# Kernel optimization log

Hardware: AMD Instinct MI355X
Metric: run time of the kernel (lower is better)

The kernel has to match this reference:

```python
import jax, jax.numpy as jnp
import numpy as np


def _gather_neighbours(h, idx):
    # h: (B, N, H); idx: (B, N, K) int -> (B, N, K, H)
    B, N, H = h.shape
    K = idx.shape[-1]
    flat = idx.reshape(B, N * K)  # (B, N*K)
    rep = jnp.take_along_axis(h, flat[..., None], axis=1)  # (B, N*K, H)
    return rep.reshape(B, N, K, H)


def _masked_agg(h, idx, mask):
    # gather neighbor hidden states then masked sum over neighbors -> (B, N, H)
    rep = _gather_neighbours(h, idx)
    return jnp.einsum('bnkh,bnk->bnh', rep, mask)


def setup_inputs() -> dict:
    key = jax.random.key(0)
    ks = jax.random.split(key, 12)
    B, N, H, K = 8, 2000, 128, 32
    s = 1.0 / np.sqrt(H)
    return {
        'node_hidden': jax.random.normal(ks[0], (B, N, H), jnp.float32),
        'cell': jax.random.normal(ks[1], (B, N, H), jnp.float32),
        'w_in': jax.random.normal(ks[2], (4, H, H), jnp.float32) * s,
        'w_out': jax.random.normal(ks[3], (4, H, H), jnp.float32) * s,
        'u_in': jax.random.normal(ks[4], (4, H, H), jnp.float32) * s,
        'u_out': jax.random.normal(ks[5], (4, H, H), jnp.float32) * s,
        'b': jax.random.normal(ks[6], (4, H), jnp.float32) * 0.1,
        'in_node_mask': jax.random.uniform(ks[7], (B, N, K), jnp.float32),
        'out_node_mask': jax.random.uniform(ks[8], (B, N, K), jnp.float32),
        'in_node_index': jax.random.randint(ks[9], (B, N, K), 0, N, jnp.int32),
        'out_node_index': jax.random.randint(ks[10], (B, N, K), 0, N, jnp.int32),
        'layer_num': 2,
    }


def reference(node_hidden, cell, w_in, w_out, u_in, u_out, b,
              in_node_mask, out_node_mask, in_node_index, out_node_index,
              layer_num):
    h, c = node_hidden, cell
    for _ in range(layer_num):
        in_agg = _masked_agg(h, in_node_index, in_node_mask)    # (B,N,H)
        out_agg = _masked_agg(h, out_node_index, out_node_mask)  # (B,N,H)
        # gate pre-activations, gate order: i, o, f, cell
        pre = (jnp.einsum('bnh,ghd->gbnd', in_agg, w_in)
               + jnp.einsum('bnh,ghd->gbnd', out_agg, w_out)
               + jnp.einsum('bnh,ghd->gbnd', h, u_in)
               + jnp.einsum('bnh,ghd->gbnd', h, u_out)
               + b[:, None, None, :])
        i_g = jax.nn.sigmoid(pre[0])
        o_g = jax.nn.sigmoid(pre[1])
        f_g = jax.nn.sigmoid(pre[2])
        g = jnp.tanh(pre[3])
        c = f_g * c + i_g * g
        h = o_g * jnp.tanh(c)
    return h
```

## Files before the change

kernel.cpp:

```cpp
#include <hip/hip_runtime.h>
#include <math.h>

#define B_ 8
#define N_ 2000
#define H_ 128
#define K_ 32
#define M_ (B_*N_)
#define KTOT 384
#define NC 512

typedef __attribute__((ext_vector_type(8))) short s8_t;
typedef __attribute__((ext_vector_type(4))) float f4_t;

__device__ __forceinline__ unsigned short f2bf(float x) {
    union { float f; unsigned u; } v; v.f = x;
    unsigned r = v.u + 0x7fff + ((v.u >> 16) & 1);
    return (unsigned short)(r >> 16);
}
__device__ __forceinline__ float bf2f(unsigned short b) {
    union { unsigned u; float f; } v; v.u = (unsigned)b << 16; return v.f;
}
__device__ __forceinline__ float sigm_(float x) { return 1.f / (1.f + __expf(-x)); }
__device__ __forceinline__ float tanh_(float x) { return 2.f / (1.f + __expf(-2.f * x)) - 1.f; }

__device__ __forceinline__ float pickv(f4_t A, int m) {
    float ab = (m & 1) ? A.y : A.x;
    float cd = (m & 1) ? A.w : A.z;
    return (m & 2) ? cd : ab;
}
__device__ __forceinline__ float pick4(float u0, float u1, float u2, float u3, int m) {
    float ab = (m & 1) ? u1 : u0;
    float cd = (m & 1) ? u3 : u2;
    return (m & 2) ? cd : ab;
}

__device__ __forceinline__ void cvt8(float4 a, float4 b, uint4& hi, uint4& lo) {
    float f[8] = {a.x, a.y, a.z, a.w, b.x, b.y, b.z, b.w};
    unsigned h[8], l[8];
    #pragma unroll
    for (int i = 0; i < 8; ++i) {
        unsigned short hs = f2bf(f[i]);
        h[i] = hs;
        l[i] = f2bf(f[i] - bf2f(hs));
    }
    hi.x = h[0] | (h[1] << 16); hi.y = h[2] | (h[3] << 16);
    hi.z = h[4] | (h[5] << 16); hi.w = h[6] | (h[7] << 16);
    lo.x = l[0] | (l[1] << 16); lo.y = l[2] | (l[3] << 16);
    lo.z = l[4] | (l[5] << 16); lo.w = l[6] | (l[7] << 16);
}

__global__ void prep_kernel(const float* __restrict__ w_in,
                            const float* __restrict__ w_out,
                            const float* __restrict__ u_in,
                            const float* __restrict__ u_out,
                            unsigned short* __restrict__ wp_hi,
                            unsigned short* __restrict__ wp_lo) {
    int j = blockIdx.x;
    int k = threadIdx.x;
    int d = j >> 2, g = j & 3;
    float v;
    if (k < 128) {
        v = w_in[(g * 128 + k) * 128 + d];
    } else if (k < 256) {
        v = w_out[(g * 128 + (k - 128)) * 128 + d];
    } else {
        int kk = k - 256;
        v = u_in[(g * 128 + kk) * 128 + d] + u_out[(g * 128 + kk) * 128 + d];
    }
    unsigned short hs = f2bf(v);
    wp_hi[(size_t)j * KTOT + k] = hs;
    wp_lo[(size_t)j * KTOT + k] = f2bf(v - bf2f(hs));
}

__global__ __launch_bounds__(256)
void agg_kernel(const float* __restrict__ h,
                const int* __restrict__ in_idx,
                const float* __restrict__ in_mask,
                const int* __restrict__ out_idx,
                const float* __restrict__ out_mask,
                unsigned short* __restrict__ agg_hi,
                unsigned short* __restrict__ agg_lo) {
    int tid = threadIdx.x;
    int r = tid >> 5;
    int t = tid & 31;
    int row = blockIdx.x * 8 + r;
    int b = row / N_;
    const float* hb = h + (size_t)b * N_ * H_;

    __shared__ int   s_idx[8][64];
    __shared__ float s_msk[8][64];
    for (int e = tid; e < 512; e += 256) {
        int r2 = e >> 6, q = e & 63;
        int ridx = blockIdx.x * 8 + r2;
        if (q < 32) {
            s_idx[r2][q] = in_idx[ridx * K_ + q];
            s_msk[r2][q] = in_mask[ridx * K_ + q];
        } else {
            s_idx[r2][q] = out_idx[ridx * K_ + (q - 32)];
            s_msk[r2][q] = out_mask[ridx * K_ + (q - 32)];
        }
    }
    __syncthreads();

    float ax = 0.f, ay = 0.f, az = 0.f, aw = 0.f;
    float ox = 0.f, oy = 0.f, oz = 0.f, ow = 0.f;
    #pragma unroll 4
    for (int k = 0; k < K_; ++k) {
        int   i1 = s_idx[r][k];
        float m1 = s_msk[r][k];
        float4 v1 = *(const float4*)(hb + (size_t)i1 * H_ + t * 4);
        int   i2 = s_idx[r][32 + k];
        float m2 = s_msk[r][32 + k];
        float4 v2 = *(const float4*)(hb + (size_t)i2 * H_ + t * 4);
        ax += m1 * v1.x; ay += m1 * v1.y; az += m1 * v1.z; aw += m1 * v1.w;
        ox += m2 * v2.x; oy += m2 * v2.y; oz += m2 * v2.z; ow += m2 * v2.w;
    }

    float fi[4] = {ax, ay, az, aw};
    float fo[4] = {ox, oy, oz, ow};
    unsigned short hi_i[4], lo_i[4], hi_o[4], lo_o[4];
    #pragma unroll
    for (int q = 0; q < 4; ++q) {
        hi_i[q] = f2bf(fi[q]); lo_i[q] = f2bf(fi[q] - bf2f(hi_i[q]));
        hi_o[q] = f2bf(fo[q]); lo_o[q] = f2bf(fo[q] - bf2f(hi_o[q]));
    }
    size_t base = (size_t)row * 256;
    *(ushort4*)(agg_hi + base + t * 4)       = make_ushort4(hi_i[0], hi_i[1], hi_i[2], hi_i[3]);
    *(ushort4*)(agg_lo + base + t * 4)       = make_ushort4(lo_i[0], lo_i[1], lo_i[2], lo_i[3]);
    *(ushort4*)(agg_hi + base + 128 + t * 4) = make_ushort4(hi_o[0], hi_o[1], hi_o[2], hi_o[3]);
    *(ushort4*)(agg_lo + base + 128 + t * 4) = make_ushort4(lo_o[0], lo_o[1], lo_o[2], lo_o[3]);
}

__global__ __launch_bounds__(256)
void gemm_gates(const unsigned short* __restrict__ agg_hi,
                const unsigned short* __restrict__ agg_lo,
                const float* __restrict__ h_src,
                const unsigned short* __restrict__ wp_hi,
                const unsigned short* __restrict__ wp_lo,
                const float* __restrict__ bias,
                const float* __restrict__ c_src,
                float* __restrict__ c_dst,
                float* __restrict__ h_dst) {
    __shared__ short As_hi[128 * 32];
    __shared__ short As_lo[128 * 32];
    __shared__ short Ws_hi[128 * 32];
    __shared__ short Ws_lo[128 * 32];

    int tid  = threadIdx.x;
    int mt   = blockIdx.x;
    int jt   = blockIdx.y;
    int row0 = mt * 128;
    int lane = tid & 63;
    int wave = tid >> 6;
    int m_off = (wave & 1) * 64;
    int n_off = (wave >> 1) * 64;
    int ml = lane & 15;
    int kg = lane >> 4;

    f4_t zero = {0.f, 0.f, 0.f, 0.f};
    f4_t acc[4][4];
    #pragma unroll
    for (int i = 0; i < 4; ++i)
        #pragma unroll
        for (int j = 0; j < 4; ++j) acc[i][j] = zero;

    int e0 = tid, e1 = tid + 256;
    int ar0 = e0 >> 2, ac0 = e0 & 3;
    int ar1 = e1 >> 2, ac1 = e1 & 3;

    #pragma unroll 1
    for (int k0 = 0; k0 < KTOT; k0 += 32) {
        uint4 ahi0, alo0, ahi1, alo1;
        if (k0 < 256) {
            const unsigned short* ph = agg_hi + (size_t)row0 * 256 + k0;
            const unsigned short* pl = agg_lo + (size_t)row0 * 256 + k0;
            ahi0 = *(const uint4*)(ph + ar0 * 256 + ac0 * 8);
            alo0 = *(const uint4*)(pl + ar0 * 256 + ac0 * 8);
            ahi1 = *(const uint4*)(ph + ar1 * 256 + ac1 * 8);
            alo1 = *(const uint4*)(pl + ar1 * 256 + ac1 * 8);
        } else {
            const float* pf = h_src + (size_t)row0 * 128 + (k0 - 256);
            float4 f0a = *(const float4*)(pf + ar0 * 128 + ac0 * 8);
            float4 f0b = *(const float4*)(pf + ar0 * 128 + ac0 * 8 + 4);
            float4 f1a = *(const float4*)(pf + ar1 * 128 + ac1 * 8);
            float4 f1b = *(const float4*)(pf + ar1 * 128 + ac1 * 8 + 4);
            cvt8(f0a, f0b, ahi0, alo0);
            cvt8(f1a, f1b, ahi1, alo1);
        }
        const unsigned short* pwh = wp_hi + (size_t)(jt * 128) * KTOT + k0;
        const unsigned short* pwl = wp_lo + (size_t)(jt * 128) * KTOT + k0;
        uint4 whi0 = *(const uint4*)(pwh + ar0 * KTOT + ac0 * 8);
        uint4 wlo0 = *(const uint4*)(pwl + ar0 * KTOT + ac0 * 8);
        uint4 whi1 = *(const uint4*)(pwh + ar1 * KTOT + ac1 * 8);
        uint4 wlo1 = *(const uint4*)(pwl + ar1 * KTOT + ac1 * 8);

        __syncthreads();
        *(uint4*)&As_hi[e0 * 8] = ahi0;
        *(uint4*)&As_hi[e1 * 8] = ahi1;
        *(uint4*)&As_lo[e0 * 8] = alo0;
        *(uint4*)&As_lo[e1 * 8] = alo1;
        *(uint4*)&Ws_hi[e0 * 8] = whi0;
        *(uint4*)&Ws_hi[e1 * 8] = whi1;
        *(uint4*)&Ws_lo[e0 * 8] = wlo0;
        *(uint4*)&Ws_lo[e1 * 8] = wlo1;
        __syncthreads();

        s8_t a_hi[4], a_lo[4], b_hi[4], b_lo[4];
        #pragma unroll
        for (int i = 0; i < 4; ++i) {
            int m = m_off + i * 16 + ml;
            a_hi[i] = *(const s8_t*)&As_hi[m * 32 + kg * 8];
            a_lo[i] = *(const s8_t*)&As_lo[m * 32 + kg * 8];
        }
        #pragma unroll
        for (int j = 0; j < 4; ++j) {
            int n = n_off + j * 16 + ml;
            b_hi[j] = *(const s8_t*)&Ws_hi[n * 32 + kg * 8];
            b_lo[j] = *(const s8_t*)&Ws_lo[n * 32 + kg * 8];
        }
        #pragma unroll
        for (int i = 0; i < 4; ++i)
            #pragma unroll
            for (int j = 0; j < 4; ++j) {
                acc[i][j] = __builtin_amdgcn_mfma_f32_16x16x32_bf16(a_hi[i], b_hi[j], acc[i][j], 0, 0, 0);
                acc[i][j] = __builtin_amdgcn_mfma_f32_16x16x32_bf16(a_hi[i], b_lo[j], acc[i][j], 0, 0, 0);
                acc[i][j] = __builtin_amdgcn_mfma_f32_16x16x32_bf16(a_lo[i], b_hi[j], acc[i][j], 0, 0, 0);
            }
    }

    int g    = lane & 3;
    int qrow = lane >> 4;
    int dl   = (lane >> 2) & 3;
    #pragma unroll
    for (int j = 0; j < 4; ++j) {
        int ncol_base = jt * 128 + n_off + j * 16;
        int d = (ncol_base >> 2) + dl;
        float b0 = bias[0 * 128 + d];
        float b1 = bias[1 * 128 + d];
        float b2 = bias[2 * 128 + d];
        float b3 = bias[3 * 128 + d];
        #pragma unroll
        for (int i = 0; i < 4; ++i) {
            f4_t A = acc[i][j];
            float s0 = pickv(A, g);
            float s1 = pickv(A, g ^ 1);
            float s2 = pickv(A, g ^ 2);
            float s3 = pickv(A, g ^ 3);
            float u0 = s0;
            float u1 = __shfl_xor(s1, 1);
            float u2 = __shfl_xor(s2, 2);
            float u3 = __shfl_xor(s3, 3);
            float p0 = pick4(u0, u1, u2, u3, g) + b0;
            float p1 = pick4(u0, u1, u2, u3, g ^ 1) + b1;
            float p2 = pick4(u0, u1, u2, u3, g ^ 2) + b2;
            float p3 = pick4(u0, u1, u2, u3, g ^ 3) + b3;
            float ig = sigm_(p0);
            float og = sigm_(p1);
            float fg = sigm_(p2);
            float cg = tanh_(p3);
            int row = row0 + m_off + i * 16 + qrow * 4 + g;
            size_t off = (size_t)row * H_ + d;
            float c_old = c_src[off];
            float c_new = fg * c_old + ig * cg;
            c_dst[off] = c_new;
            h_dst[off] = og * tanh_(c_new);
        }
    }
}

extern "C" void kernel_launch(void* const* d_in, const int* in_sizes, int n_in,
                              void* d_out, int out_size, void* d_ws, size_t ws_size,
                              hipStream_t stream) {
    const float* node_hidden = (const float*)d_in[0];
    const float* cell        = (const float*)d_in[1];
    const float* w_in        = (const float*)d_in[2];
    const float* w_out       = (const float*)d_in[3];
    const float* u_in        = (const float*)d_in[4];
    const float* u_out       = (const float*)d_in[5];
    const float* bias        = (const float*)d_in[6];
    const float* in_mask     = (const float*)d_in[7];
    const float* out_mask    = (const float*)d_in[8];
    const int*   in_idx      = (const int*)d_in[9];
    const int*   out_idx     = (const int*)d_in[10];
    float* out = (float*)d_out;

    char* p = (char*)d_ws;
    unsigned short* wp_hi  = (unsigned short*)p;                     p += (size_t)NC * KTOT * 2;
    unsigned short* wp_lo  = (unsigned short*)p;                     p += (size_t)NC * KTOT * 2;
    unsigned short* agg_hi = (unsigned short*)p;                     p += (size_t)M_ * 256 * 2;
    unsigned short* agg_lo = (unsigned short*)p;                     p += (size_t)M_ * 256 * 2;
    float* h_buf = (float*)p;                                        p += (size_t)M_ * H_ * 4;
    float* c_buf = (float*)p;                                        p += (size_t)M_ * H_ * 4;

    prep_kernel<<<NC, KTOT, 0, stream>>>(w_in, w_out, u_in, u_out, wp_hi, wp_lo);

    agg_kernel<<<M_ / 8, 256, 0, stream>>>(node_hidden, in_idx, in_mask,
                                           out_idx, out_mask, agg_hi, agg_lo);
    gemm_gates<<<dim3(M_ / 128, 4), 256, 0, stream>>>(
        agg_hi, agg_lo, node_hidden, wp_hi, wp_lo, bias, cell, c_buf, h_buf);

    agg_kernel<<<M_ / 8, 256, 0, stream>>>(h_buf, in_idx, in_mask,
                                           out_idx, out_mask, agg_hi, agg_lo);
    gemm_gates<<<dim3(M_ / 128, 4), 256, 0, stream>>>(
        agg_hi, agg_lo, h_buf, wp_hi, wp_lo, bias, c_buf, c_buf, out);
}
```

Measured before the change: 205.8 us.

## Fuse neighbour aggregation and gate GEMM into one per-layer kernel

Merges the gather-aggregate kernel and the gate GEMM into a single kernel per layer. Each 32-row block aggregates in/out neighbours and h into LDS as split bf16 hi/lo, then multiplies against all 512 gate columns. Weights are prepacked into the MFMA fragment order so they can be read straight from global memory without LDS staging. This removes the global round trip of the aggregated activations and two launches, in exchange for smaller M tiles, weight traffic repeated across 500 blocks, and higher register pressure.

```diff
diff --git a/kernel.cpp b/kernel.cpp
--- a/kernel.cpp
+++ b/kernel.cpp
@@ -8,6 +8,8 @@
 #define M_ (B_*N_)
 #define KTOT 384
 #define NC 512
+#define NTILES 32
+#define NCHUNK 12
 
 typedef __attribute__((ext_vector_type(8))) short s8_t;
 typedef __attribute__((ext_vector_type(4))) float f4_t;
@@ -34,8 +36,7 @@
     return (m & 2) ? cd : ab;
 }
 
-__device__ __forceinline__ void cvt8(float4 a, float4 b, uint4& hi, uint4& lo) {
-    float f[8] = {a.x, a.y, a.z, a.w, b.x, b.y, b.z, b.w};
+__device__ __forceinline__ void split_store(short* ph, short* pl, const float* f) {
     unsigned h[8], l[8];
     #pragma unroll
     for (int i = 0; i < 8; ++i) {
@@ -43,21 +44,29 @@
         h[i] = hs;
         l[i] = f2bf(f[i] - bf2f(hs));
     }
-    hi.x = h[0] | (h[1] << 16); hi.y = h[2] | (h[3] << 16);
-    hi.z = h[4] | (h[5] << 16); hi.w = h[6] | (h[7] << 16);
-    lo.x = l[0] | (l[1] << 16); lo.y = l[2] | (l[3] << 16);
-    lo.z = l[4] | (l[5] << 16); lo.w = l[6] | (l[7] << 16);
-}
-
-__global__ void prep_kernel(const float* __restrict__ w_in,
-                            const float* __restrict__ w_out,
-                            const float* __restrict__ u_in,
-                            const float* __restrict__ u_out,
-                            unsigned short* __restrict__ wp_hi,
-                            unsigned short* __restrict__ wp_lo) {
-    int j = blockIdx.x;
-    int k = threadIdx.x;
-    int d = j >> 2, g = j & 3;
+    uint4 H, L;
+    H.x = h[0] | (h[1] << 16); H.y = h[2] | (h[3] << 16);
+    H.z = h[4] | (h[5] << 16); H.w = h[6] | (h[7] << 16);
+    L.x = l[0] | (l[1] << 16); L.y = l[2] | (l[3] << 16);
+    L.z = l[4] | (l[5] << 16); L.w = l[6] | (l[7] << 16);
+    *(uint4*)ph = H;
+    *(uint4*)pl = L;
+}
+
+__global__ __launch_bounds__(512)
+void prep_kernel(const float* __restrict__ w_in,
+                 const float* __restrict__ w_out,
+                 const float* __restrict__ u_in,
+                 const float* __restrict__ u_out,
+                 unsigned short* __restrict__ wp_hi,
+                 unsigned short* __restrict__ wp_lo) {
+    int blk = blockIdx.x;
+    int ntile = blk / NCHUNK, chunk = blk % NCHUNK;
+    int t = threadIdx.x;
+    int lane = t >> 3, e = t & 7;
+    int col = ntile * 16 + (lane & 15);
+    int k = chunk * 32 + (lane >> 4) * 8 + e;
+    int d = col >> 2, g = col & 3;
     float v;
     if (k < 128) {
         v = w_in[(g * 128 + k) * 128 + d];
@@ -68,164 +77,109 @@
         v = u_in[(g * 128 + kk) * 128 + d] + u_out[(g * 128 + kk) * 128 + d];
     }
     unsigned short hs = f2bf(v);
-    wp_hi[(size_t)j * KTOT + k] = hs;
-    wp_lo[(size_t)j * KTOT + k] = f2bf(v - bf2f(hs));
-}
-
-__global__ __launch_bounds__(256)
-void agg_kernel(const float* __restrict__ h,
-                const int* __restrict__ in_idx,
-                const float* __restrict__ in_mask,
-                const int* __restrict__ out_idx,
-                const float* __restrict__ out_mask,
-                unsigned short* __restrict__ agg_hi,
-                unsigned short* __restrict__ agg_lo) {
+    wp_hi[(size_t)blk * 512 + t] = hs;
+    wp_lo[(size_t)blk * 512 + t] = f2bf(v - bf2f(hs));
+}
+
+__global__ __launch_bounds__(512, 4)
+void fused_layer(const float* __restrict__ h_src,
+                 const int* __restrict__ in_idx,
+                 const float* __restrict__ in_mask,
+                 const int* __restrict__ out_idx,
+                 const float* __restrict__ out_mask,
+                 const unsigned short* __restrict__ wp_hi,
+                 const unsigned short* __restrict__ wp_lo,
+                 const float* __restrict__ bias,
+                 const float* __restrict__ c_src,
+                 float* __restrict__ c_dst,
+                 float* __restrict__ h_dst) {
+    __shared__ short As_hi[NCHUNK * 32 * 32];
+    __shared__ short As_lo[NCHUNK * 32 * 32];
+
     int tid = threadIdx.x;
-    int r = tid >> 5;
-    int t = tid & 31;
-    int row = blockIdx.x * 8 + r;
-    int b = row / N_;
-    const float* hb = h + (size_t)b * N_ * H_;
-
-    __shared__ int   s_idx[8][64];
-    __shared__ float s_msk[8][64];
-    for (int e = tid; e < 512; e += 256) {
-        int r2 = e >> 6, q = e & 63;
-        int ridx = blockIdx.x * 8 + r2;
-        if (q < 32) {
-            s_idx[r2][q] = in_idx[ridx * K_ + q];
-            s_msk[r2][q] = in_mask[ridx * K_ + q];
-        } else {
-            s_idx[r2][q] = out_idx[ridx * K_ + (q - 32)];
-            s_msk[r2][q] = out_mask[ridx * K_ + (q - 32)];
-        }
+    int row0 = blockIdx.x * 32;
+
+    {
+        int r = tid >> 4;
+        int p = tid & 15;
+        int d0 = p * 8;
+        int row = row0 + r;
+        int b = row / N_;
+        const float* hb = h_src + (size_t)b * N_ * H_;
+        const int*   pii = in_idx  + (size_t)row * K_;
+        const float* pim = in_mask + (size_t)row * K_;
+        const int*   poi = out_idx + (size_t)row * K_;
+        const float* pom = out_mask + (size_t)row * K_;
+
+        float ai[8] = {0,0,0,0,0,0,0,0};
+        float ao[8] = {0,0,0,0,0,0,0,0};
+        #pragma unroll 4
+        for (int k = 0; k < K_; ++k) {
+            int   ii = pii[k];
+            float mi = pim[k];
+            int   oi = poi[k];
+            float mo = pom[k];
+            const float* pv = hb + (size_t)ii * H_ + d0;
+            const float* pw = hb + (size_t)oi * H_ + d0;
+            float4 v0 = *(const float4*)pv;
+            float4 v1 = *(const float4*)(pv + 4);
+            float4 w0 = *(const float4*)pw;
+            float4 w1 = *(const float4*)(pw + 4);
+            ai[0] += mi * v0.x; ai[1] += mi * v0.y; ai[2] += mi * v0.z; ai[3] += mi * v0.w;
+            ai[4] += mi * v1.x; ai[5] += mi * v1.y; ai[6] += mi * v1.z; ai[7] += mi * v1.w;
+            ao[0] += mo * w0.x; ao[1] += mo * w0.y; ao[2] += mo * w0.z; ao[3] += mo * w0.w;
+            ao[4] += mo * w1.x; ao[5] += mo * w1.y; ao[6] += mo * w1.z; ao[7] += mo * w1.w;
+        }
+        const float* ph = h_src + (size_t)row * H_ + d0;
+        float4 u0 = *(const float4*)ph;
+        float4 u1 = *(const float4*)(ph + 4);
+        float hh[8] = {u0.x, u0.y, u0.z, u0.w, u1.x, u1.y, u1.z, u1.w};
+
+        int ci  = p >> 2;
+        int off = (p & 3) * 8;
+        int base_in = ((ci)     * 32 + r) * 32 + off;
+        int base_ou = ((4 + ci) * 32 + r) * 32 + off;
+        int base_hh = ((8 + ci) * 32 + r) * 32 + off;
+        split_store(&As_hi[base_in], &As_lo[base_in], ai);
+        split_store(&As_hi[base_ou], &As_lo[base_ou], ao);
+        split_store(&As_hi[base_hh], &As_lo[base_hh], hh);
     }
     __syncthreads();
 
-    float ax = 0.f, ay = 0.f, az = 0.f, aw = 0.f;
-    float ox = 0.f, oy = 0.f, oz = 0.f, ow = 0.f;
-    #pragma unroll 4
-    for (int k = 0; k < K_; ++k) {
-        int   i1 = s_idx[r][k];
-        float m1 = s_msk[r][k];
-        float4 v1 = *(const float4*)(hb + (size_t)i1 * H_ + t * 4);
-        int   i2 = s_idx[r][32 + k];
-        float m2 = s_msk[r][32 + k];
-        float4 v2 = *(const float4*)(hb + (size_t)i2 * H_ + t * 4);
-        ax += m1 * v1.x; ay += m1 * v1.y; az += m1 * v1.z; aw += m1 * v1.w;
-        ox += m2 * v2.x; oy += m2 * v2.y; oz += m2 * v2.z; ow += m2 * v2.w;
-    }
-
-    float fi[4] = {ax, ay, az, aw};
-    float fo[4] = {ox, oy, oz, ow};
-    unsigned short hi_i[4], lo_i[4], hi_o[4], lo_o[4];
-    #pragma unroll
-    for (int q = 0; q < 4; ++q) {
-        hi_i[q] = f2bf(fi[q]); lo_i[q] = f2bf(fi[q] - bf2f(hi_i[q]));
-        hi_o[q] = f2bf(fo[q]); lo_o[q] = f2bf(fo[q] - bf2f(hi_o[q]));
-    }
-    size_t base = (size_t)row * 256;
-    *(ushort4*)(agg_hi + base + t * 4)       = make_ushort4(hi_i[0], hi_i[1], hi_i[2], hi_i[3]);
-    *(ushort4*)(agg_lo + base + t * 4)       = make_ushort4(lo_i[0], lo_i[1], lo_i[2], lo_i[3]);
-    *(ushort4*)(agg_hi + base + 128 + t * 4) = make_ushort4(hi_o[0], hi_o[1], hi_o[2], hi_o[3]);
-    *(ushort4*)(agg_lo + base + 128 + t * 4) = make_ushort4(lo_o[0], lo_o[1], lo_o[2], lo_o[3]);
-}
-
-__global__ __launch_bounds__(256)
-void gemm_gates(const unsigned short* __restrict__ agg_hi,
-                const unsigned short* __restrict__ agg_lo,
-                const float* __restrict__ h_src,
-                const unsigned short* __restrict__ wp_hi,
-                const unsigned short* __restrict__ wp_lo,
-                const float* __restrict__ bias,
-                const float* __restrict__ c_src,
-                float* __restrict__ c_dst,
-                float* __restrict__ h_dst) {
-    __shared__ short As_hi[128 * 32];
-    __shared__ short As_lo[128 * 32];
-    __shared__ short Ws_hi[128 * 32];
-    __shared__ short Ws_lo[128 * 32];
-
-    int tid  = threadIdx.x;
-    int mt   = blockIdx.x;
-    int jt   = blockIdx.y;
-    int row0 = mt * 128;
     int lane = tid & 63;
-    int wave = tid >> 6;
-    int m_off = (wave & 1) * 64;
-    int n_off = (wave >> 1) * 64;
+    int w = tid >> 6;
     int ml = lane & 15;
     int kg = lane >> 4;
 
     f4_t zero = {0.f, 0.f, 0.f, 0.f};
-    f4_t acc[4][4];
+    f4_t acc[2][4];
     #pragma unroll
-    for (int i = 0; i < 4; ++i)
+    for (int i = 0; i < 2; ++i)
         #pragma unroll
         for (int j = 0; j < 4; ++j) acc[i][j] = zero;
 
-    int e0 = tid, e1 = tid + 256;
-    int ar0 = e0 >> 2, ac0 = e0 & 3;
-    int ar1 = e1 >> 2, ac1 = e1 & 3;
-
-    #pragma unroll 1
-    for (int k0 = 0; k0 < KTOT; k0 += 32) {
-        uint4 ahi0, alo0, ahi1, alo1;
-        if (k0 < 256) {
-            const unsigned short* ph = agg_hi + (size_t)row0 * 256 + k0;
-            const unsigned short* pl = agg_lo + (size_t)row0 * 256 + k0;
-            ahi0 = *(const uint4*)(ph + ar0 * 256 + ac0 * 8);
-            alo0 = *(const uint4*)(pl + ar0 * 256 + ac0 * 8);
-            ahi1 = *(const uint4*)(ph + ar1 * 256 + ac1 * 8);
-            alo1 = *(const uint4*)(pl + ar1 * 256 + ac1 * 8);
-        } else {
-            const float* pf = h_src + (size_t)row0 * 128 + (k0 - 256);
-            float4 f0a = *(const float4*)(pf + ar0 * 128 + ac0 * 8);
-            float4 f0b = *(const float4*)(pf + ar0 * 128 + ac0 * 8 + 4);
-            float4 f1a = *(const float4*)(pf + ar1 * 128 + ac1 * 8);
-            float4 f1b = *(const float4*)(pf + ar1 * 128 + ac1 * 8 + 4);
-            cvt8(f0a, f0b, ahi0, alo0);
-            cvt8(f1a, f1b, ahi1, alo1);
-        }
-        const unsigned short* pwh = wp_hi + (size_t)(jt * 128) * KTOT + k0;
-        const unsigned short* pwl = wp_lo + (size_t)(jt * 128) * KTOT + k0;
-        uint4 whi0 = *(const uint4*)(pwh + ar0 * KTOT + ac0 * 8);
-        uint4 wlo0 = *(const uint4*)(pwl + ar0 * KTOT + ac0 * 8);
-        uint4 whi1 = *(const uint4*)(pwh + ar1 * KTOT + ac1 * 8);
-        uint4 wlo1 = *(const uint4*)(pwl + ar1 * KTOT + ac1 * 8);
-
-        __syncthreads();
-        *(uint4*)&As_hi[e0 * 8] = ahi0;
-        *(uint4*)&As_hi[e1 * 8] = ahi1;
-        *(uint4*)&As_lo[e0 * 8] = alo0;
-        *(uint4*)&As_lo[e1 * 8] = alo1;
-        *(uint4*)&Ws_hi[e0 * 8] = whi0;
-        *(uint4*)&Ws_hi[e1 * 8] = whi1;
-        *(uint4*)&Ws_lo[e0 * 8] = wlo0;
-        *(uint4*)&Ws_lo[e1 * 8] = wlo1;
-        __syncthreads();
-
-        s8_t a_hi[4], a_lo[4], b_hi[4], b_lo[4];
-        #pragma unroll
-        for (int i = 0; i < 4; ++i) {
-            int m = m_off + i * 16 + ml;
-            a_hi[i] = *(const s8_t*)&As_hi[m * 32 + kg * 8];
-            a_lo[i] = *(const s8_t*)&As_lo[m * 32 + kg * 8];
+    int w4 = w * 4;
+    #pragma unroll 2
+    for (int c = 0; c < NCHUNK; ++c) {
+        s8_t a_hi[2], a_lo[2];
+        #pragma unroll
+        for (int i = 0; i < 2; ++i) {
+            int m = i * 16 + ml;
+            a_hi[i] = *(const s8_t*)&As_hi[(c * 32 + m) * 32 + kg * 8];
+            a_lo[i] = *(const s8_t*)&As_lo[(c * 32 + m) * 32 + kg * 8];
         }
         #pragma unroll
         for (int j = 0; j < 4; ++j) {
-            int n = n_off + j * 16 + ml;
-            b_hi[j] = *(const s8_t*)&Ws_hi[n * 32 + kg * 8];
-            b_lo[j] = *(const s8_t*)&Ws_lo[n * 32 + kg * 8];
-        }
-        #pragma unroll
-        for (int i = 0; i < 4; ++i)
+            size_t boff = (((size_t)(w4 + j) * NCHUNK + c) * 64 + lane) * 8;
+            s8_t b_hi = *(const s8_t*)(wp_hi + boff);
+            s8_t b_lo = *(const s8_t*)(wp_lo + boff);
             #pragma unroll
-            for (int j = 0; j < 4; ++j) {
-                acc[i][j] = __builtin_amdgcn_mfma_f32_16x16x32_bf16(a_hi[i], b_hi[j], acc[i][j], 0, 0, 0);
-                acc[i][j] = __builtin_amdgcn_mfma_f32_16x16x32_bf16(a_hi[i], b_lo[j], acc[i][j], 0, 0, 0);
-                acc[i][j] = __builtin_amdgcn_mfma_f32_16x16x32_bf16(a_lo[i], b_hi[j], acc[i][j], 0, 0, 0);
+            for (int i = 0; i < 2; ++i) {
+                acc[i][j] = __builtin_amdgcn_mfma_f32_16x16x32_bf16(a_hi[i], b_hi, acc[i][j], 0, 0, 0);
+                acc[i][j] = __builtin_amdgcn_mfma_f32_16x16x32_bf16(a_hi[i], b_lo, acc[i][j], 0, 0, 0);
+                acc[i][j] = __builtin_amdgcn_mfma_f32_16x16x32_bf16(a_lo[i], b_hi, acc[i][j], 0, 0, 0);
             }
+        }
     }
 
     int g    = lane & 3;
@@ -233,14 +187,14 @@
     int dl   = (lane >> 2) & 3;
     #pragma unroll
     for (int j = 0; j < 4; ++j) {
-        int ncol_base = jt * 128 + n_off + j * 16;
+        int ncol_base = w * 64 + j * 16;
         int d = (ncol_base >> 2) + dl;
         float b0 = bias[0 * 128 + d];
         float b1 = bias[1 * 128 + d];
         float b2 = bias[2 * 128 + d];
         float b3 = bias[3 * 128 + d];
         #pragma unroll
-        for (int i = 0; i < 4; ++i) {
+        for (int i = 0; i < 2; ++i) {
             f4_t A = acc[i][j];
             float s0 = pickv(A, g);
             float s1 = pickv(A, g ^ 1);
@@ -258,7 +212,7 @@
             float og = sigm_(p1);
             float fg = sigm_(p2);
             float cg = tanh_(p3);
-            int row = row0 + m_off + i * 16 + qrow * 4 + g;
+            int row = row0 + i * 16 + qrow * 4 + g;
             size_t off = (size_t)row * H_ + d;
             float c_old = c_src[off];
             float c_new = fg * c_old + ig * cg;
@@ -285,22 +239,18 @@
     float* out = (float*)d_out;
 
     char* p = (char*)d_ws;
-    unsigned short* wp_hi  = (unsigned short*)p;                     p += (size_t)NC * KTOT * 2;
-    unsigned short* wp_lo  = (unsigned short*)p;                     p += (size_t)NC * KTOT * 2;
-    unsigned short* agg_hi = (unsigned short*)p;                     p += (size_t)M_ * 256 * 2;
-    unsigned short* agg_lo = (unsigned short*)p;                     p += (size_t)M_ * 256 * 2;
-    float* h_buf = (float*)p;                                        p += (size_t)M_ * H_ * 4;
-    float* c_buf = (float*)p;                                        p += (size_t)M_ * H_ * 4;
-
-    prep_kernel<<<NC, KTOT, 0, stream>>>(w_in, w_out, u_in, u_out, wp_hi, wp_lo);
-
-    agg_kernel<<<M_ / 8, 256, 0, stream>>>(node_hidden, in_idx, in_mask,
-                                           out_idx, out_mask, agg_hi, agg_lo);
-    gemm_gates<<<dim3(M_ / 128, 4), 256, 0, stream>>>(
-        agg_hi, agg_lo, node_hidden, wp_hi, wp_lo, bias, cell, c_buf, h_buf);
-
-    agg_kernel<<<M_ / 8, 256, 0, stream>>>(h_buf, in_idx, in_mask,
-                                           out_idx, out_mask, agg_hi, agg_lo);
-    gemm_gates<<<dim3(M_ / 128, 4), 256, 0, stream>>>(
-        agg_hi, agg_lo, h_buf, wp_hi, wp_lo, bias, c_buf, c_buf, out);
-}
+    unsigned short* wp_hi = (unsigned short*)p; p += (size_t)NTILES * NCHUNK * 512 * 2;
+    unsigned short* wp_lo = (unsigned short*)p; p += (size_t)NTILES * NCHUNK * 512 * 2;
+    float* h_buf = (float*)p;                   p += (size_t)M_ * H_ * 4;
+    float* c_buf = (float*)p;                   p += (size_t)M_ * H_ * 4;
+
+    prep_kernel<<<NTILES * NCHUNK, 512, 0, stream>>>(w_in, w_out, u_in, u_out, wp_hi, wp_lo);
+
+    fused_layer<<<M_ / 32, 512, 0, stream>>>(
+        node_hidden, in_idx, in_mask, out_idx, out_mask,
+        wp_hi, wp_lo, bias, cell, c_buf, h_buf);
+
+    fused_layer<<<M_ / 32, 512, 0, stream>>>(
+        h_buf, in_idx, in_mask, out_idx, out_mask,
+        wp_hi, wp_lo, bias, c_buf, c_buf, out);
+}
```

Result: slower. 217.8 us (+5.8%).
